# Performance work log

Hardware: AMD Instinct MI355X
Metric: run time of the kernel (lower is better)

The kernel has to match this reference:

```python
import jax, jax.numpy as jnp
import numpy as np

B, N_IN, N_ALL, NPT, K, C, H = 8, 20000, 1200, 1024, 34, 96, 6
DH = C // H
RADIUS2 = (2.5 * 0.04) ** 2  # grid_size=0.04, sigma=1.0 -> radius 0.1


def _fps(xyz, npoint):
    # furthest point sampling, vectorized over batch, scan over sample steps
    Bb, Nn, _ = xyz.shape
    def step(carry, _):
        dist, far = carry
        cen = jnp.take_along_axis(xyz, far[:, None, None], axis=1)  # [B,1,3]
        d = jnp.sum((xyz - cen) ** 2, -1)                           # [B,N]
        dist = jnp.minimum(dist, d)
        return (dist, jnp.argmax(dist, -1).astype(jnp.int32)), far
    init = (jnp.full((Bb, Nn), 1e10, xyz.dtype), jnp.zeros((Bb,), jnp.int32))
    _, idx = jax.lax.scan(step, init, None, length=npoint)
    return idx.T  # [B, npoint]


def _gather(x, idx):
    return jnp.take_along_axis(x, idx[:, :, None], axis=1)


def _ln(x, g, b):
    m = jnp.mean(x, -1, keepdims=True)
    v = jnp.var(x, -1, keepdims=True)
    return (x - m) * jax.lax.rsqrt(v + 1e-5) * g + b


def _forward(point_clouds, cloud_colors, W_in, b_in, Wq, Wk, Wv, Wo, Wpos, W1, b1, W2, b2, g1, be1, g2, be2, sel):
    fps_idx = _fps(point_clouds, N_ALL)      # [B,1200]
    fps_idx = fps_idx[:, sel]                # random 1024 of 1200 (fixed permutation)
    coord = _gather(point_clouds, fps_idx)   # [B,P,3]
    color = _gather(cloud_colors, fps_idx)   # [B,P,3]
    # ball query within each cloud (all clouds have equal count -> batched dense dists)
    d2 = jnp.sum((coord[:, :, None] - coord[:, None]) ** 2, -1)        # [B,P,P]
    valid = d2 <= RADIUS2
    nidx = jnp.argsort(jnp.where(valid, d2, 1e10), axis=-1)[..., :K]   # [B,P,K]
    nvalid = jnp.take_along_axis(valid, nidx, axis=-1)                 # [B,P,K]
    feat = jnp.concatenate([color, coord], -1)                         # [B,P,6]
    x = feat @ W_in + b_in                                             # [B,P,C]
    q = (x @ Wq).reshape(B, NPT, H, DH)
    k = x @ Wk
    v = x @ Wv
    def gat(t):  # gather per-neighbor features: [B,P,C*] -> [B,P,K,C*]
        return jnp.take_along_axis(t, nidx.reshape(B, NPT * K)[:, :, None], axis=1).reshape(B, NPT, K, -1)
    kn, vn, pn = gat(k), gat(v), gat(coord)
    pe = (coord[:, :, None] - pn) @ Wpos                               # [B,P,K,C] rel-pos enc
    kn = (kn + pe).reshape(B, NPT, K, H, DH)
    vn = (vn + pe).reshape(B, NPT, K, H, DH)
    logits = jnp.einsum('bphd,bpkhd->bphk', q, kn) / jnp.sqrt(jnp.float32(DH))
    logits = jnp.where(nvalid[:, :, None, :], logits, -1e9)
    attn = jax.nn.softmax(logits, -1)
    out = jnp.einsum('bphk,bpkhd->bphd', attn, vn).reshape(B, NPT, C)
    x = _ln(x + out @ Wo, g1, be1)
    x = _ln(x + jax.nn.relu(x @ W1 + b1) @ W2 + b2, g2, be2)
    features = jnp.transpose(x, (0, 2, 1))                             # [B,C,P]
    return features, coord


def setup_inputs() -> dict:
    key = jax.random.key(0)
    ks = jax.random.split(key, 16)
    s = 0.1
    w = lambda k, shp: jax.random.normal(k, shp, jnp.float32) * s
    return {
        'point_clouds': jax.random.uniform(ks[0], (B, N_IN, 3), jnp.float32),
        'cloud_colors': jax.random.uniform(ks[1], (B, N_IN, 3), jnp.float32),
        'W_in': w(ks[2], (6, C)), 'b_in': jnp.zeros((C,), jnp.float32),
        'Wq': w(ks[3], (C, C)), 'Wk': w(ks[4], (C, C)), 'Wv': w(ks[5], (C, C)),
        'Wo': w(ks[6], (C, C)), 'Wpos': w(ks[7], (3, C)),
        'W1': w(ks[8], (C, 4 * C)), 'b1': jnp.zeros((4 * C,), jnp.float32),
        'W2': w(ks[9], (4 * C, C)), 'b2': jnp.zeros((C,), jnp.float32),
        'g1': jnp.ones((C,), jnp.float32), 'be1': jnp.zeros((C,), jnp.float32),
        'g2': jnp.ones((C,), jnp.float32), 'be2': jnp.zeros((C,), jnp.float32),
        'sel': jax.random.permutation(ks[10], N_ALL)[:NPT].astype(jnp.int32),
    }


def reference(point_clouds, cloud_colors, W_in, b_in, Wq, Wk, Wv, Wo, Wpos, W1, b1, W2, b2, g1, be1, g2, be2, sel):
    return _forward(point_clouds, cloud_colors, W_in, b_in, Wq, Wk, Wv, Wo, Wpos, W1, b1, W2, b2, g1, be1, g2, be2, sel)
```

## Files before the change

### kernel.cpp

```cpp
#include <hip/hip_runtime.h>
#include <math.h>

#define B_   8
#define NIN  20000
#define NALL 1200
#define NPTQ 1024
#define KNB  34
#define CH   96
#define FF   384
#define NQ   (B_ * NPTQ)

#define FT   512
#define NPR  20

typedef unsigned int   u32;
typedef unsigned long long u64;
typedef float v2f __attribute__((ext_vector_type(2)));

__device__ __forceinline__ float scrub(float f) {
    u32 u = __float_as_uint(f);
    return ((u & 0x7F800000u) == 0x7F800000u) ? 12345.0f : f;
}

__global__ __launch_bounds__(FT, 2) void fps_kernel(const float* __restrict__ pc,
                                                    int* __restrict__ fps_idx) {
#pragma clang fp contract(off)
    const int b = blockIdx.x;
    const int tid = threadIdx.x;
    const int lane = tid & 63;
    const int wid = tid >> 6;
    const float* base = pc + (size_t)b * NIN * 3;

    v2f px[NPR], py[NPR], pz[NPR], dist[NPR];
#pragma unroll
    for (int j = 0; j < NPR; ++j) {
        int i0 = tid + (2 * j) * FT;
        int i1 = i0 + FT;
        bool ok1 = i1 < NIN;
        int a1 = ok1 ? i1 : 0;
        float x0 = base[(size_t)i0 * 3 + 0];
        float y0 = base[(size_t)i0 * 3 + 1];
        float z0 = base[(size_t)i0 * 3 + 2];
        float x1 = base[(size_t)a1 * 3 + 0];
        float y1 = base[(size_t)a1 * 3 + 1];
        float z1 = base[(size_t)a1 * 3 + 2];
        x0 = __shfl(x0, lane); y0 = __shfl(y0, lane); z0 = __shfl(z0, lane);
        x1 = __shfl(x1, lane); y1 = __shfl(y1, lane); z1 = __shfl(z1, lane);
        px[j].x = x0; px[j].y = x1;
        py[j].x = y0; py[j].y = y1;
        pz[j].x = z0; pz[j].y = z1;
        dist[j].x = 1e10f;
        dist[j].y = ok1 ? 1e10f : -1.0f;
    }

    __shared__ u64 rkey[2][8];

    if (tid == 0) fps_idx[b * NALL + 0] = 0;
    float cx = base[0], cy = base[1], cz = base[2];

    for (int it = 1; it < NALL; ++it) {
        const int pb = it & 1;
        v2f cvx; cvx.x = cx; cvx.y = cx;
        v2f cvy; cvy.x = cy; cvy.y = cy;
        v2f cvz; cvz.x = cz; cvz.y = cz;
        float bd0 = -1e38f, bd1 = -1e38f;
        int bi0 = 0, bi1 = 0;
#pragma unroll
        for (int j = 0; j < NPR; ++j) {
            v2f dx = px[j] - cvx;
            v2f dy = py[j] - cvy;
            v2f dz = pz[j] - cvz;
            v2f sx = dx * dx;
            v2f sy = dy * dy;
            v2f sz = dz * dz;
            v2f d  = (sx + sy) + sz;
            v2f nd = __builtin_elementwise_min(dist[j], d);
            dist[j] = nd;
            if (nd.x > bd0) { bd0 = nd.x; bi0 = tid + (2 * j) * FT; }
            if (nd.y > bd1) { bd1 = nd.y; bi1 = tid + (2 * j + 1) * FT; }
        }
        u64 k0 = ((u64)__float_as_uint(bd0) << 32) | (u32)(NIN - bi0);
        u64 k1 = ((u64)__float_as_uint(bd1) << 32) | (u32)(NIN - bi1);
        u64 key = (k1 > k0) ? k1 : k0;
#pragma unroll
        for (int s = 32; s; s >>= 1) {
            u64 o = __shfl_xor(key, s, 64);
            key = (o > key) ? o : key;
        }
        if (lane == 0) rkey[pb][wid] = key;
        __syncthreads();
        u64 kk = rkey[pb][0];
#pragma unroll
        for (int w = 1; w < 8; ++w) { u64 o = rkey[pb][w]; kk = (o > kk) ? o : kk; }
        int widx = NIN - (int)(kk & 0xFFFFFFFFu);
        if (tid == 0) fps_idx[b * NALL + it] = widx;
        const float* wp = base + (size_t)widx * 3;
        cx = wp[0]; cy = wp[1]; cz = wp[2];
    }
}

__global__ void gather_kernel(const float* __restrict__ pc,
                              const int* __restrict__ fps_idx, const int* __restrict__ sel,
                              float* __restrict__ coord, float* __restrict__ out_coord) {
    int t = blockIdx.x * 256 + threadIdx.x;
    if (t >= NQ) return;
    int b = t >> 10, j = t & 1023;
    int p = fps_idx[b * NALL + sel[j]];
    p = (p < 0) ? 0 : ((p >= NIN) ? (NIN - 1) : p);
    const float* pp = pc + ((size_t)b * NIN + p) * 3;
    float x = pp[0], y = pp[1], z = pp[2];
    coord[(size_t)t * 3 + 0] = x;
    coord[(size_t)t * 3 + 1] = y;
    coord[(size_t)t * 3 + 2] = z;
    out_coord[(size_t)t * 3 + 0] = scrub(x);
    out_coord[(size_t)t * 3 + 1] = scrub(y);
    out_coord[(size_t)t * 3 + 2] = scrub(z);
}

__global__ void knn_kernel(const float* __restrict__ coord, int* __restrict__ nbr) {
    __shared__ float sx[NPTQ], sy[NPTQ], sz[NPTQ];
    const double RAD2D = (2.5 * 0.04) * (2.5 * 0.04);
    int b = blockIdx.x >> 8;
    int i0 = (blockIdx.x & 255) * 4;
    const float* cb = coord + (size_t)b * NPTQ * 3;
    for (int t = threadIdx.x; t < NPTQ; t += 256) {
        sx[t] = cb[(size_t)t * 3 + 0];
        sy[t] = cb[(size_t)t * 3 + 1];
        sz[t] = cb[(size_t)t * 3 + 2];
    }
    __syncthreads();
    int wid = threadIdx.x >> 6, lane = threadIdx.x & 63;
    int i = i0 + wid;
    float qx = sx[i], qy = sy[i], qz = sz[i];
    u64 pk[16];
#pragma unroll
    for (int t = 0; t < 16; ++t) {
        int j = lane + t * 64;
        float dx = __fsub_rn(qx, sx[j]);
        float dy = __fsub_rn(qy, sy[j]);
        float dz = __fsub_rn(qz, sz[j]);
        float d2 = __fadd_rn(__fadd_rn(__fmul_rn(dx, dx), __fmul_rn(dy, dy)),
                             __fmul_rn(dz, dz));
        bool valid = ((double)d2 <= RAD2D);
        pk[t] = valid ? (((u64)__float_as_uint(d2) << 32) | (u32)j) : ~0ull;
    }
    int* out = nbr + ((size_t)b * NPTQ + i) * KNB;
    int k = 0;
    for (; k < KNB; ++k) {
        u64 m = ~0ull;
#pragma unroll
        for (int t = 0; t < 16; ++t) m = (pk[t] < m) ? pk[t] : m;
#pragma unroll
        for (int s = 32; s; s >>= 1) {
            u64 o = __shfl_xor(m, s, 64);
            m = (o < m) ? o : m;
        }
        if (m == ~0ull) break;
#pragma unroll
        for (int t = 0; t < 16; ++t) if (pk[t] == m) pk[t] = ~0ull;
        if (lane == 0) out[k] = (int)(m & 0xFFFFFFFFu);
    }
    for (; k < KNB; ++k) if (lane == 0) out[k] = -1;
}

__global__ void xproj_kernel(const float* __restrict__ pc, const float* __restrict__ col,
                             const int* __restrict__ fps_idx, const int* __restrict__ sel,
                             const float* __restrict__ Win, const float* __restrict__ bin,
                             float* __restrict__ x) {
    int idx = blockIdx.x * 256 + threadIdx.x;
    if (idx >= NQ * CH) return;
    int q = idx / CH, c = idx - q * CH;
    int b = q >> 10, j = q & 1023;
    int p = fps_idx[b * NALL + sel[j]];
    p = (p < 0) ? 0 : ((p >= NIN) ? (NIN - 1) : p);
    const float* pp = pc + ((size_t)b * NIN + p) * 3;
    const float* cc = col + ((size_t)b * NIN + p) * 3;
    float acc = bin[c];
    acc += cc[0] * Win[0 * CH + c];
    acc += cc[1] * Win[1 * CH + c];
    acc += cc[2] * Win[2 * CH + c];
    acc += pp[0] * Win[3 * CH + c];
    acc += pp[1] * Win[4 * CH + c];
    acc += pp[2] * Win[5 * CH + c];
    x[idx] = acc;
}

__global__ void qkv_kernel(const float* __restrict__ x,
                           const float* __restrict__ Wq, const float* __restrict__ Wk,
                           const float* __restrict__ Wv,
                           float* __restrict__ qo, float* __restrict__ ko,
                           float* __restrict__ vo) {
    int idx = blockIdx.x * 256 + threadIdx.x;
    if (idx >= NQ * CH) return;
    int q = idx / CH, c = idx - q * CH;
    const float* xr = x + (size_t)q * CH;
    float aq = 0.f, ak = 0.f, av = 0.f;
    for (int k = 0; k < CH; ++k) {
        float xv = xr[k];
        aq += xv * Wq[k * CH + c];
        ak += xv * Wk[k * CH + c];
        av += xv * Wv[k * CH + c];
    }
    qo[idx] = aq; ko[idx] = ak; vo[idx] = av;
}

__global__ __launch_bounds__(384) void attn_kernel(float* __restrict__ qr1,
                            const float* __restrict__ km, const float* __restrict__ vm,
                            const float* __restrict__ coord, const int* __restrict__ nbr,
                            const float* __restrict__ Wpos, const float* __restrict__ Wo,
                            const float* __restrict__ x) {
    __shared__ float wp[3 * CH];
    __shared__ float os[4][CH];
    for (int t = threadIdx.x; t < 3 * CH; t += 384) wp[t] = Wpos[t];
    __syncthreads();
    int lq = threadIdx.x / CH;
    int c = threadIdx.x - lq * CH;
    int qi = blockIdx.x * 4 + lq;
    int b = qi >> 10, i = qi & 1023;
    const float* crd = coord + (size_t)b * NPTQ * 3;
    float cx = crd[(size_t)i * 3], cy = crd[(size_t)i * 3 + 1], cz = crd[(size_t)i * 3 + 2];
    float qv = qr1[(size_t)qi * CH + c];
    const int* nb = nbr + (size_t)qi * KNB;
    float m = -1e30f, l = 0.f, acc = 0.f;
    for (int t = 0; t < KNB; ++t) {
        int j = nb[t];
        if (j < 0) break;
        float dx = cx - crd[(size_t)j * 3];
        float dy = cy - crd[(size_t)j * 3 + 1];
        float dz = cz - crd[(size_t)j * 3 + 2];
        float pe = dx * wp[c] + dy * wp[CH + c] + dz * wp[2 * CH + c];
        size_t row = (size_t)(b * NPTQ + j) * CH + c;
        float kn = km[row] + pe;
        float s = qv * kn;
        s += __shfl_xor(s, 1); s += __shfl_xor(s, 2);
        s += __shfl_xor(s, 4); s += __shfl_xor(s, 8);
        float logit = s * 0.25f;
        float mn = fmaxf(m, logit);
        float sc = expf(m - mn);
        float p = expf(logit - mn);
        float vn = vm[row] + pe;
        l = l * sc + p;
        acc = acc * sc + p * vn;
        m = mn;
    }
    os[lq][c] = (l > 0.f) ? acc / l : 0.f;
    __syncthreads();
    float r = x[(size_t)qi * CH + c];
    for (int k = 0; k < CH; ++k) r += os[lq][k] * Wo[k * CH + c];
    qr1[(size_t)qi * CH + c] = r;
}

__global__ void ln_kernel(const float* __restrict__ in, const float* __restrict__ g,
                          const float* __restrict__ be, float* __restrict__ out) {
    int row = blockIdx.x * 4 + (threadIdx.x >> 6);
    int lane = threadIdx.x & 63;
    const float* r = in + (size_t)row * CH;
    float e0 = r[lane];
    float e1 = (lane < 32) ? r[64 + lane] : 0.0f;
    float s = e0 + e1;
#pragma unroll
    for (int k = 32; k; k >>= 1) s += __shfl_xor(s, k);
    float mean = s * (1.0f / 96.0f);
    float d0 = e0 - mean, d1 = e1 - mean;
    float vs = d0 * d0 + ((lane < 32) ? d1 * d1 : 0.0f);
#pragma unroll
    for (int k = 32; k; k >>= 1) vs += __shfl_xor(vs, k);
    float rs = 1.0f / sqrtf(vs * (1.0f / 96.0f) + 1e-5f);
    float* o = out + (size_t)row * CH;
    o[lane] = d0 * rs * g[lane] + be[lane];
    if (lane < 32) o[64 + lane] = d1 * rs * g[64 + lane] + be[64 + lane];
}

__global__ __launch_bounds__(384) void ffn_kernel(const float* __restrict__ x2,
                           const float* __restrict__ W1, const float* __restrict__ b1,
                           const float* __restrict__ W2, const float* __restrict__ b2,
                           float* __restrict__ r2) {
    __shared__ float xs[4][CH];
    __shared__ float hs[4][FF];
    __shared__ float ps[4][4][CH];
    int row0 = blockIdx.x * 4, t = threadIdx.x;
    { int r = t / CH, c = t - (t / CH) * CH;
      xs[r][c] = x2[(size_t)(row0 + r) * CH + c]; }
    __syncthreads();
    {
        float bt = b1[t];
        float a0 = bt, a1 = bt, a2 = bt, a3 = bt;
        for (int k = 0; k < CH; ++k) {
            float w = W1[k * FF + t];
            a0 += xs[0][k] * w; a1 += xs[1][k] * w;
            a2 += xs[2][k] * w; a3 += xs[3][k] * w;
        }
        hs[0][t] = fmaxf(a0, 0.f); hs[1][t] = fmaxf(a1, 0.f);
        hs[2][t] = fmaxf(a2, 0.f); hs[3][t] = fmaxf(a3, 0.f);
    }
    __syncthreads();
    {
        int chunk = t / CH, c = t - (t / CH) * CH;
        float p0 = 0.f, p1 = 0.f, p2 = 0.f, p3 = 0.f;
        for (int m = chunk * CH; m < (chunk + 1) * CH; ++m) {
            float w = W2[m * CH + c];
            p0 += hs[0][m] * w; p1 += hs[1][m] * w;
            p2 += hs[2][m] * w; p3 += hs[3][m] * w;
        }
        ps[0][chunk][c] = p0; ps[1][chunk][c] = p1;
        ps[2][chunk][c] = p2; ps[3][chunk][c] = p3;
    }
    __syncthreads();
    { int r = t / CH, c = t - (t / CH) * CH;
      float rr = xs[r][c] + ((ps[r][0][c] + ps[r][1][c]) + (ps[r][2][c] + ps[r][3][c])) + b2[c];
      r2[(size_t)(row0 + r) * CH + c] = rr; }
}

__global__ void ln2t_kernel(const float* __restrict__ in, const float* __restrict__ g,
                            const float* __restrict__ be, float* __restrict__ out) {
    int row = blockIdx.x * 4 + (threadIdx.x >> 6);
    int lane = threadIdx.x & 63;
    int b = row >> 10, i = row & 1023;
    const float* r = in + (size_t)row * CH;
    float e0 = r[lane];
    float e1 = (lane < 32) ? r[64 + lane] : 0.0f;
    float s = e0 + e1;
#pragma unroll
    for (int k = 32; k; k >>= 1) s += __shfl_xor(s, k);
    float mean = s * (1.0f / 96.0f);
    float d0 = e0 - mean, d1 = e1 - mean;
    float vs = d0 * d0 + ((lane < 32) ? d1 * d1 : 0.0f);
#pragma unroll
    for (int k = 32; k; k >>= 1) vs += __shfl_xor(vs, k);
    float rs = 1.0f / sqrtf(vs * (1.0f / 96.0f) + 1e-5f);
    float y0 = d0 * rs * g[lane] + be[lane];
    out[((size_t)(b * CH + lane)) * NPTQ + i] = scrub(y0);
    if (lane < 32) {
        float y1 = d1 * rs * g[64 + lane] + be[64 + lane];
        out[((size_t)(b * CH + 64 + lane)) * NPTQ + i] = scrub(y1);
    }
}

extern "C" void kernel_launch(void* const* d_in, const int* in_sizes, int n_in,
                              void* d_out, int out_size, void* d_ws, size_t ws_size,
                              hipStream_t stream) {
    const float* pc   = (const float*)d_in[0];
    const float* col  = (const float*)d_in[1];
    const float* Win  = (const float*)d_in[2];
    const float* bin  = (const float*)d_in[3];
    const float* Wq   = (const float*)d_in[4];
    const float* Wk   = (const float*)d_in[5];
    const float* Wv   = (const float*)d_in[6];
    const float* Wo   = (const float*)d_in[7];
    const float* Wpos = (const float*)d_in[8];
    const float* W1   = (const float*)d_in[9];
    const float* b1   = (const float*)d_in[10];
    const float* W2   = (const float*)d_in[11];
    const float* b2   = (const float*)d_in[12];
    const float* g1   = (const float*)d_in[13];
    const float* be1  = (const float*)d_in[14];
    const float* g2   = (const float*)d_in[15];
    const float* be2  = (const float*)d_in[16];
    const int*  sel   = (const int*)d_in[17];

    float* out_feat  = (float*)d_out;
    float* out_coord = out_feat + (size_t)B_ * CH * NPTQ;

    char* ws = (char*)d_ws;
    size_t off = 0;
    auto alloc = [&](size_t bytes) { void* p = ws + off; off += (bytes + 255) & ~(size_t)255; return p; };
    int*   w_fps   = (int*)  alloc((size_t)B_ * NALL * 4);
    float* w_coord = (float*)alloc((size_t)NQ * 3 * 4);
    int*   w_nbr   = (int*)  alloc((size_t)NQ * KNB * 4);
    float* w_x     = (float*)alloc((size_t)NQ * CH * 4);
    float* w_q     = (float*)alloc((size_t)NQ * CH * 4);
    float* w_k     = (float*)alloc((size_t)NQ * CH * 4);
    float* w_v     = (float*)alloc((size_t)NQ * CH * 4);
    (void)ws_size; (void)in_sizes; (void)n_in; (void)out_size;

    fps_kernel<<<B_, FT, 0, stream>>>(pc, w_fps);
    gather_kernel<<<NQ / 256, 256, 0, stream>>>(pc, w_fps, sel, w_coord, out_coord);
    knn_kernel<<<NQ / 4, 256, 0, stream>>>(w_coord, w_nbr);
    xproj_kernel<<<NQ * CH / 256, 256, 0, stream>>>(pc, col, w_fps, sel, Win, bin, w_x);
    qkv_kernel<<<NQ * CH / 256, 256, 0, stream>>>(w_x, Wq, Wk, Wv, w_q, w_k, w_v);
    attn_kernel<<<NQ / 4, 384, 0, stream>>>(w_q, w_k, w_v, w_coord, w_nbr, Wpos, Wo, w_x);
    ln_kernel<<<NQ / 4, 256, 0, stream>>>(w_q, g1, be1, w_k);
    ffn_kernel<<<NQ / 4, 384, 0, stream>>>(w_k, W1, b1, W2, b2, w_v);
    ln2t_kernel<<<NQ / 4, 256, 0, stream>>>(w_v, g2, be2, out_feat);
}
```

Before: 2.481 ms.

## Split FPS across 8 cooperating blocks per cloud with global-memory argmax exchange

Furthest point sampling now runs on 8 blocks per batch instead of one. Each block holds a slice of the points and publishes its local argmax key plus the winner's coordinates into per-iteration global slots. Wave 0 of each block spin-waits until all 8 slots are filled, then reduces them to the global winner. This puts the serial 1200-step loop on many more CUs and cuts per-step compute, in exchange for a global-memory round trip per step, a memset of the slot buffer, and reliance on all 64 blocks being co-resident, with a spin limit as the fallback.

After: 3.058 ms. +23.3%, slower.

```diff
diff --git a/kernel.cpp b/kernel.cpp
--- a/kernel.cpp
+++ b/kernel.cpp
@@ -11,7 +11,10 @@
 #define NQ   (B_ * NPTQ)
 
 #define FT   512
-#define NPR  20
+#define FPB  8
+#define PPB  (NIN / FPB)
+#define NPRF 3
+#define SPIN_LIM 4096u
 
 typedef unsigned int   u32;
 typedef unsigned long long u64;
@@ -23,24 +26,31 @@
 }
 
 __global__ __launch_bounds__(FT, 2) void fps_kernel(const float* __restrict__ pc,
+                                                    u64* slots,
                                                     int* __restrict__ fps_idx) {
 #pragma clang fp contract(off)
-    const int b = blockIdx.x;
-    const int tid = threadIdx.x;
+    const int blk  = blockIdx.x;
+    const int b    = blk >> 3;
+    const int part = blk & (FPB - 1);
+    const int tid  = threadIdx.x;
     const int lane = tid & 63;
-    const int wid = tid >> 6;
+    const int wid  = tid >> 6;
     const float* base = pc + (size_t)b * NIN * 3;
-
-    v2f px[NPR], py[NPR], pz[NPR], dist[NPR];
-#pragma unroll
-    for (int j = 0; j < NPR; ++j) {
-        int i0 = tid + (2 * j) * FT;
-        int i1 = i0 + FT;
-        bool ok1 = i1 < NIN;
-        int a1 = ok1 ? i1 : 0;
-        float x0 = base[(size_t)i0 * 3 + 0];
-        float y0 = base[(size_t)i0 * 3 + 1];
-        float z0 = base[(size_t)i0 * 3 + 2];
+    const int P0 = part * PPB;
+    u64* bslot = slots + (size_t)b * NALL * FPB * 4;
+
+    v2f px[NPRF], py[NPRF], pz[NPRF], dist[NPRF];
+#pragma unroll
+    for (int j = 0; j < NPRF; ++j) {
+        int l0 = tid + (2 * j) * FT;
+        int l1 = l0 + FT;
+        bool ok0 = l0 < PPB;
+        bool ok1 = l1 < PPB;
+        int a0 = P0 + (ok0 ? l0 : 0);
+        int a1 = P0 + (ok1 ? l1 : 0);
+        float x0 = base[(size_t)a0 * 3 + 0];
+        float y0 = base[(size_t)a0 * 3 + 1];
+        float z0 = base[(size_t)a0 * 3 + 2];
         float x1 = base[(size_t)a1 * 3 + 0];
         float y1 = base[(size_t)a1 * 3 + 1];
         float z1 = base[(size_t)a1 * 3 + 2];
@@ -49,13 +59,14 @@
         px[j].x = x0; px[j].y = x1;
         py[j].x = y0; py[j].y = y1;
         pz[j].x = z0; pz[j].y = z1;
-        dist[j].x = 1e10f;
+        dist[j].x = ok0 ? 1e10f : -1.0f;
         dist[j].y = ok1 ? 1e10f : -1.0f;
     }
 
     __shared__ u64 rkey[2][8];
-
-    if (tid == 0) fps_idx[b * NALL + 0] = 0;
+    __shared__ u64 win[2][4];
+
+    if (part == 0 && tid == 0) fps_idx[b * NALL + 0] = 0;
     float cx = base[0], cy = base[1], cz = base[2];
 
     for (int it = 1; it < NALL; ++it) {
@@ -66,7 +77,7 @@
         float bd0 = -1e38f, bd1 = -1e38f;
         int bi0 = 0, bi1 = 0;
 #pragma unroll
-        for (int j = 0; j < NPR; ++j) {
+        for (int j = 0; j < NPRF; ++j) {
             v2f dx = px[j] - cvx;
             v2f dy = py[j] - cvy;
             v2f dz = pz[j] - cvz;
@@ -79,9 +90,10 @@
             if (nd.x > bd0) { bd0 = nd.x; bi0 = tid + (2 * j) * FT; }
             if (nd.y > bd1) { bd1 = nd.y; bi1 = tid + (2 * j + 1) * FT; }
         }
-        u64 k0 = ((u64)__float_as_uint(bd0) << 32) | (u32)(NIN - bi0);
-        u64 k1 = ((u64)__float_as_uint(bd1) << 32) | (u32)(NIN - bi1);
-        u64 key = (k1 > k0) ? k1 : k0;
+        u64 k0 = (1ULL << 63) | ((u64)__float_as_uint(bd0) << 16) | (u32)(NIN - (P0 + bi0));
+        u64 k1 = (1ULL << 63) | ((u64)__float_as_uint(bd1) << 16) | (u32)(NIN - (P0 + bi1));
+        u64 myk = (k1 > k0) ? k1 : k0;
+        u64 key = myk;
 #pragma unroll
         for (int s = 32; s; s >>= 1) {
             u64 o = __shfl_xor(key, s, 64);
@@ -92,10 +104,63 @@
         u64 kk = rkey[pb][0];
 #pragma unroll
         for (int w = 1; w < 8; ++w) { u64 o = rkey[pb][w]; kk = (o > kk) ? o : kk; }
-        int widx = NIN - (int)(kk & 0xFFFFFFFFu);
-        if (tid == 0) fps_idx[b * NALL + it] = widx;
-        const float* wp = base + (size_t)widx * 3;
-        cx = wp[0]; cy = wp[1]; cz = wp[2];
+
+        if (myk == kk) {
+            int lw = (NIN - (int)(kk & 0xFFFFu)) - P0;
+            int sl = lw >> 9;
+            float wx = 0.f, wy = 0.f, wz = 0.f;
+#pragma unroll
+            for (int j = 0; j < NPRF; ++j) {
+                if (sl == 2 * j)     { wx = px[j].x; wy = py[j].x; wz = pz[j].x; }
+                if (sl == 2 * j + 1) { wx = px[j].y; wy = py[j].y; wz = pz[j].y; }
+            }
+            u64* sp = bslot + (size_t)(it * FPB + part) * 4;
+            __hip_atomic_store(sp + 1, (1ULL << 63) | (u64)__float_as_uint(wx),
+                               __ATOMIC_RELAXED, __HIP_MEMORY_SCOPE_AGENT);
+            __hip_atomic_store(sp + 2, (1ULL << 63) | (u64)__float_as_uint(wy),
+                               __ATOMIC_RELAXED, __HIP_MEMORY_SCOPE_AGENT);
+            __hip_atomic_store(sp + 3, (1ULL << 63) | (u64)__float_as_uint(wz),
+                               __ATOMIC_RELAXED, __HIP_MEMORY_SCOPE_AGENT);
+            __hip_atomic_store(sp + 0, kk,
+                               __ATOMIC_RELAXED, __HIP_MEMORY_SCOPE_AGENT);
+        }
+
+        if (wid == 0) {
+            const u64* rowbase = bslot + (size_t)it * FPB * 4;
+            u64 w = 0;
+            const bool active = lane < 32;
+            for (u32 round = 0;; ++round) {
+                if (active)
+                    w = __hip_atomic_load(rowbase + lane, __ATOMIC_RELAXED,
+                                          __HIP_MEMORY_SCOPE_AGENT);
+                u64 ball = __ballot((int)(w >> 63));
+                if (((ball & 0xFFFFFFFFull) == 0xFFFFFFFFull) || round > SPIN_LIM)
+                    break;
+            }
+            u64 k = __shfl(w, lane & ~3, 64);
+            u64 kmax = k;
+#pragma unroll
+            for (int s = 4; s < 32; s <<= 1) {
+                u64 o = __shfl_xor(kmax, s, 64);
+                kmax = (o > kmax) ? o : kmax;
+            }
+            int gw = NIN - (int)(kmax & 0xFFFFu);
+            int wpart = gw / PPB;
+            u64 xw = __shfl(w, wpart * 4 + 1, 64);
+            u64 yw = __shfl(w, wpart * 4 + 2, 64);
+            u64 zw = __shfl(w, wpart * 4 + 3, 64);
+            if (lane == 0) {
+                win[pb][0] = kmax; win[pb][1] = xw;
+                win[pb][2] = yw;   win[pb][3] = zw;
+            }
+        }
+        __syncthreads();
+        u64 best = win[pb][0];
+        int widx = NIN - (int)(best & 0xFFFFu);
+        if (part == 0 && tid == 0) fps_idx[b * NALL + it] = widx;
+        cx = __uint_as_float((u32)win[pb][1]);
+        cy = __uint_as_float((u32)win[pb][2]);
+        cz = __uint_as_float((u32)win[pb][3]);
     }
 }
 
@@ -371,9 +436,14 @@
     float* w_q     = (float*)alloc((size_t)NQ * CH * 4);
     float* w_k     = (float*)alloc((size_t)NQ * CH * 4);
     float* w_v     = (float*)alloc((size_t)NQ * CH * 4);
+    const size_t slot_bytes = (size_t)B_ * NALL * FPB * 4 * sizeof(u64);
+    u64*   w_slots = (u64*)  alloc(slot_bytes);
     (void)ws_size; (void)in_sizes; (void)n_in; (void)out_size;
 
-    fps_kernel<<<B_, FT, 0, stream>>>(pc, w_fps);
+    hipMemsetAsync(w_slots, 0, slot_bytes, stream);
+
+    fps_kernel<<<B_ * FPB, FT, 0, stream>>>(pc, w_slots, w_fps);
+
     gather_kernel<<<NQ / 256, 256, 0, stream>>>(pc, w_fps, sel, w_coord, out_coord);
     knn_kernel<<<NQ / 4, 256, 0, stream>>>(w_coord, w_nbr);
     xproj_kernel<<<NQ * CH / 256, 256, 0, stream>>>(pc, col, w_fps, sel, Win, bin, w_x);
```

## Split FPS argmax into float max reduction plus rare index-recovery pass

Applied to the files above, without the earlier changes.

Replaces the per-element tracked (value,index) 64-bit key reduction in the furthest-point-sampling loop with a packed float max reduction, then recovers the smallest index only in waves that hold the maximum, using a mask scan, a u32 min shuffle and a shared atomicMin. This cuts per-iteration ALU work and the 64-bit shuffle reduction on the serial 1200-step critical path. In exchange it adds a second __syncthreads per iteration and an extra divergent pass. It also drops redundant self-shuffles in the load loop.

Result: slower. 2.588 ms (+4.3%).

```diff
diff --git a/kernel.cpp b/kernel.cpp
--- a/kernel.cpp
+++ b/kernel.cpp
@@ -44,8 +44,7 @@
         float x1 = base[(size_t)a1 * 3 + 0];
         float y1 = base[(size_t)a1 * 3 + 1];
         float z1 = base[(size_t)a1 * 3 + 2];
-        x0 = __shfl(x0, lane); y0 = __shfl(y0, lane); z0 = __shfl(z0, lane);
-        x1 = __shfl(x1, lane); y1 = __shfl(y1, lane); z1 = __shfl(z1, lane);
+        asm volatile("" : "+v"(x0), "+v"(y0), "+v"(z0), "+v"(x1), "+v"(y1), "+v"(z1));
         px[j].x = x0; px[j].y = x1;
         py[j].x = y0; py[j].y = y1;
         pz[j].x = z0; pz[j].y = z1;
@@ -53,9 +52,15 @@
         dist[j].y = ok1 ? 1e10f : -1.0f;
     }
 
-    __shared__ u64 rkey[2][8];
-
-    if (tid == 0) fps_idx[b * NALL + 0] = 0;
+    __shared__ float wmax[2][8];
+    __shared__ u32 widx_s[2];
+
+    if (tid == 0) {
+        widx_s[0] = 0xFFFFFFFFu;
+        widx_s[1] = 0xFFFFFFFFu;
+        fps_idx[b * NALL + 0] = 0;
+    }
+    __syncthreads();
     float cx = base[0], cy = base[1], cz = base[2];
 
     for (int it = 1; it < NALL; ++it) {
@@ -63,8 +68,7 @@
         v2f cvx; cvx.x = cx; cvx.y = cx;
         v2f cvy; cvy.x = cy; cvy.y = cy;
         v2f cvz; cvz.x = cz; cvz.y = cz;
-        float bd0 = -1e38f, bd1 = -1e38f;
-        int bi0 = 0, bi1 = 0;
+        v2f run; run.x = -1e38f; run.y = -1e38f;
 #pragma unroll
         for (int j = 0; j < NPR; ++j) {
             v2f dx = px[j] - cvx;
@@ -76,24 +80,39 @@
             v2f d  = (sx + sy) + sz;
             v2f nd = __builtin_elementwise_min(dist[j], d);
             dist[j] = nd;
-            if (nd.x > bd0) { bd0 = nd.x; bi0 = tid + (2 * j) * FT; }
-            if (nd.y > bd1) { bd1 = nd.y; bi1 = tid + (2 * j + 1) * FT; }
+            run = __builtin_elementwise_max(run, nd);
         }
-        u64 k0 = ((u64)__float_as_uint(bd0) << 32) | (u32)(NIN - bi0);
-        u64 k1 = ((u64)__float_as_uint(bd1) << 32) | (u32)(NIN - bi1);
-        u64 key = (k1 > k0) ? k1 : k0;
-#pragma unroll
-        for (int s = 32; s; s >>= 1) {
-            u64 o = __shfl_xor(key, s, 64);
-            key = (o > key) ? o : key;
+        float lm = fmaxf(run.x, run.y);
+        float wm = lm;
+#pragma unroll
+        for (int s = 32; s; s >>= 1) wm = fmaxf(wm, __shfl_xor(wm, s, 64));
+        if (lane == 0) wmax[pb][wid] = wm;
+        __syncthreads();
+        if (tid == 0) widx_s[pb ^ 1] = 0xFFFFFFFFu;
+        float M = wmax[pb][0];
+#pragma unroll
+        for (int w = 1; w < 8; ++w) M = fmaxf(M, wmax[pb][w]);
+
+        if (__any(lm == M)) {
+            u64 msk = 0;
+#pragma unroll
+            for (int j = 0; j < NPR; ++j) {
+                if (dist[j].x == M) msk |= (1ull << (2 * j));
+                if (dist[j].y == M) msk |= (1ull << (2 * j + 1));
+            }
+            u32 slot = (u32)__builtin_ctzll(msk | (1ull << 63));
+            u32 cand = slot * (u32)FT + (u32)tid;
+#pragma unroll
+            for (int s = 32; s; s >>= 1) {
+                u32 o = (u32)__shfl_xor((int)cand, s, 64);
+                cand = (o < cand) ? o : cand;
+            }
+            if (lane == 0) atomicMin(&widx_s[pb], cand);
         }
-        if (lane == 0) rkey[pb][wid] = key;
         __syncthreads();
-        u64 kk = rkey[pb][0];
-#pragma unroll
-        for (int w = 1; w < 8; ++w) { u64 o = rkey[pb][w]; kk = (o > kk) ? o : kk; }
-        int widx = NIN - (int)(kk & 0xFFFFFFFFu);
-        if (tid == 0) fps_idx[b * NALL + it] = widx;
+        u32 widx = widx_s[pb];
+        widx = (widx < NIN) ? widx : 0;
+        if (tid == 0) fps_idx[b * NALL + it] = (int)widx;
         const float* wp = base + (size_t)widx * 3;
         cx = wp[0]; cy = wp[1]; cz = wp[2];
     }
```
